# Kernel optimization log

Hardware: AMD Instinct MI355X
Metric: run time of the kernel (lower is better)

The kernel has to match this reference:

```python
import jax, jax.numpy as jnp
import numpy as np

B, T, F, H, L = 128, 256, 128, 768, 2


def lstm_cell(x, h, c, Wih, Whh, b):
    # torch gate order: i, f, g, o
    gates = x @ Wih.T + h @ Whh.T + b
    i, f, g, o = jnp.split(gates, 4, axis=-1)
    i = jax.nn.sigmoid(i)
    f = jax.nn.sigmoid(f)
    g = jnp.tanh(g)
    o = jax.nn.sigmoid(o)
    c2 = f * c + i * g
    h2 = o * jnp.tanh(c2)
    return h2, c2


def setup_inputs() -> dict:
    key = jax.random.key(0)
    ks = jax.random.split(key, 20)
    k_scale = 1.0 / np.sqrt(H)

    def U(k, shape):
        return jax.random.uniform(k, shape, jnp.float32, -k_scale, k_scale)

    inp = {
        "x": jax.random.normal(ks[0], (B, T, F), jnp.float32),
        "h0": jax.random.normal(ks[1], (L, B, H), jnp.float32),
        "c0": jax.random.normal(ks[2], (L, B, H), jnp.float32),
        # encoder LSTM (layer 0 input dim F, layer 1 input dim H); b = b_ih + b_hh fused
        "enc_Wih0": U(ks[3], (4 * H, F)),
        "enc_Whh0": U(ks[4], (4 * H, H)),
        "enc_b0": U(ks[5], (4 * H,)),
        "enc_Wih1": U(ks[6], (4 * H, H)),
        "enc_Whh1": U(ks[7], (4 * H, H)),
        "enc_b1": U(ks[8], (4 * H,)),
        # decoder LSTM
        "dec_Wih0": U(ks[9], (4 * H, F)),
        "dec_Whh0": U(ks[10], (4 * H, H)),
        "dec_b0": U(ks[11], (4 * H,)),
        "dec_Wih1": U(ks[12], (4 * H, H)),
        "dec_Whh1": U(ks[13], (4 * H, H)),
        "dec_b1": U(ks[14], (4 * H,)),
        # output projection hidden -> feature
        "lin_W": U(ks[15], (F, H)),
        "lin_b": U(ks[16], (F,)),
    }
    return inp


def reference(x, h0, c0,
              enc_Wih0, enc_Whh0, enc_b0, enc_Wih1, enc_Whh1, enc_b1,
              dec_Wih0, dec_Whh0, dec_b0, dec_Wih1, dec_Whh1, dec_b1,
              lin_W, lin_b):
    # ---- Encoder: 2-layer LSTM over full sequence, keep final (h, c) ----
    xs = jnp.transpose(x, (1, 0, 2))  # [T, B, F]

    def enc_step(carry, xt):
        (h_l0, h_l1), (c_l0, c_l1) = carry
        h0n, c0n = lstm_cell(xt, h_l0, c_l0, enc_Wih0, enc_Whh0, enc_b0)
        h1n, c1n = lstm_cell(h0n, h_l1, c_l1, enc_Wih1, enc_Whh1, enc_b1)
        return ((h0n, h1n), (c0n, c1n)), None

    enc_init = ((h0[0], h0[1]), (c0[0], c0[1]))
    (h_fin, c_fin), _ = jax.lax.scan(enc_step, enc_init, xs)

    x_dec0 = x[:, -1, :]  # [B, F]

    def dec_step(carry, _):
        (h_l0, h_l1), (c_l0, c_l1), xd = carry
        h0n, c0n = lstm_cell(xd, h_l0, c_l0, dec_Wih0, dec_Whh0, dec_b0)
        h1n, c1n = lstm_cell(h0n, h_l1, c_l1, dec_Wih1, dec_Whh1, dec_b1)
        y = h1n @ lin_W.T + lin_b  # [B, F]
        return (((h0n, h1n), (c0n, c1n), y)), y

    dec_init = (h_fin, c_fin, x_dec0)
    _, ys = jax.lax.scan(dec_step, dec_init, None, length=T)  # [T, B, F]

    # decoder step t writes output index T-1-t -> reversed time order
    out = jnp.transpose(jnp.flip(ys, axis=0), (1, 0, 2))  # [B, T, F]
    return out
```

## Files before the change

kernel.cpp:

```cpp
#include <hip/hip_runtime.h>

#define B_ 128
#define T_ 256
#define F_ 128
#define H_ 768
#define NG 3072
#define BM 32
#define BN 64
#define BK 128
#define UPT 16

typedef short s16x8 __attribute__((ext_vector_type(8)));
typedef float f32x4 __attribute__((ext_vector_type(4)));

__device__ __forceinline__ unsigned short f2bf(float x) {
  unsigned u = __float_as_uint(x);
  u += 0x7fffu + ((u >> 16) & 1u);
  return (unsigned short)(u >> 16);
}

__device__ __forceinline__ void async16(const void* g, void* l) {
  __builtin_amdgcn_global_load_lds(
      (const __attribute__((address_space(1))) void*)g,
      (__attribute__((address_space(3))) void*)l, 16, 0, 0);
}

struct Cell {
  const unsigned short* A1; int lda1; int K1;
  const unsigned short* A2; int lda2; int K2;
  const unsigned short* W;  int ldw;
  const float* bias;
  float* c;
  unsigned short* h;
  float* yout; int yt;
  int N; int ngates;
};

__global__ __launch_bounds__(256, 2) void cell_kernel(Cell ca, Cell cb, int mode)
{
  __shared__ union SM {
    struct { unsigned short A[3][BM*BK]; unsigned short Bm[3][BN*BK]; } stg;
    float gates[BM][BN+4];
  } sm;

  const int bid = (int)blockIdx.x;
  int tm, tn; bool isB = false;
  if (mode == 0) {
    int xcd = bid & 7, j = bid >> 3;
    isB = j >= 24; int jj = isB ? j - 24 : j;
    tn = xcd * 6 + (jj >> 2); tm = jj & 3;
  } else if (mode == 1) {
    int xcd = bid & 7, j = bid >> 3;
    if (j < 24) { tn = xcd * 6 + (j >> 2); tm = j & 3; }
    else        { tn = 48 + (xcd >> 2); tm = xcd & 3; }
  } else if (mode == 2) {
    int xcd = bid & 7, j = bid >> 3;
    tn = xcd * 6 + (j >> 2); tm = j & 3;
  } else {
    tm = bid & 3; tn = bid >> 2;
  }
  const Cell C = isB ? cb : ca;
  const int b0 = tm * BM;

  const int tid  = (int)threadIdx.x;
  const int wave = tid >> 6;
  const int lane = tid & 63;
  const int wm = wave >> 1, wn = wave & 1;

  const int nit = (C.K1 + C.K2) / BK;

  f32x4 acc[2] = {{0.f,0.f,0.f,0.f},{0.f,0.f,0.f,0.f}};

  auto stage = [&](int buf, int ck) {
    int kk = ck * BK;
#pragma unroll
    for (int q = 0; q < 2; ++q) {
      int cch = wave*2 + q;
      int P = cch*1024 + lane*16;
      int r = P >> 8;
      int sl = ((P >> 4) & 15) ^ (r & 7);
      int ke = kk + sl*8;
      const unsigned short* gp = (ke < C.K1)
        ? (C.A1 + (long)(b0 + r) * C.lda1 + ke)
        : (C.A2 + (long)(b0 + r) * C.lda2 + (ke - C.K1));
      async16(gp, (char*)(sm.stg.A[buf]) + cch*1024);
    }
#pragma unroll
    for (int q = 0; q < 4; ++q) {
      int cch = wave*4 + q;
      int P = cch*1024 + lane*16;
      int r = P >> 8;
      int sl = ((P >> 4) & 15) ^ (r & 7);
      int ke = kk + sl*8;
      const unsigned short* gp = C.W + (long)(tn*BN + r) * C.ldw + ke;
      async16(gp, (char*)(sm.stg.Bm[buf]) + cch*1024);
    }
  };

  auto compute = [&](int buf) {
    const char* At = (const char*)(sm.stg.A[buf]);
    const char* Bt = (const char*)(sm.stg.Bm[buf]);
#pragma unroll
    for (int ks = 0; ks < 4; ++ks) {
      int ar = wm*16 + (lane & 15);
      int as = (ks*4 + (lane >> 4)) ^ (ar & 7);
      s16x8 a = *(const s16x8*)(At + ar*256 + as*16);
#pragma unroll
      for (int nf = 0; nf < 2; ++nf) {
        int br = wn*32 + nf*16 + (lane & 15);
        int bsl = (ks*4 + (lane >> 4)) ^ (br & 7);
        s16x8 b = *(const s16x8*)(Bt + br*256 + bsl*16);
        acc[nf] = __builtin_amdgcn_mfma_f32_16x16x32_bf16(a, b, acc[nf], 0, 0, 0);
      }
    }
  };

  stage(0, 0);
  stage(1, 1);
  for (int it = 0; it < nit; ++it) {
    if (it + 1 < nit) asm volatile("s_waitcnt vmcnt(6)" ::: "memory");
    else              asm volatile("s_waitcnt vmcnt(0)" ::: "memory");
    __builtin_amdgcn_s_barrier();
    __builtin_amdgcn_sched_barrier(0);
    if (it + 2 < nit) stage((it + 2) % 3, it + 2);
    compute(it % 3);
  }

  const int gcol0 = tn * BN;
  if (gcol0 >= C.ngates) {
#pragma unroll
    for (int nf = 0; nf < 2; ++nf) {
      int col = wn*32 + nf*16 + (lane & 15);
      float bia = C.bias[gcol0 + col];
      int fo = gcol0 + col - C.ngates;
#pragma unroll
      for (int rg = 0; rg < 4; ++rg) {
        int brow = wm*16 + (lane >> 4)*4 + rg;
        C.yout[(long)(b0 + brow)*(T_*F_) + (long)C.yt*F_ + fo] = acc[nf][rg] + bia;
      }
    }
    return;
  }

  __syncthreads();
#pragma unroll
  for (int nf = 0; nf < 2; ++nf) {
    int col = wn*32 + nf*16 + (lane & 15);
#pragma unroll
    for (int rg = 0; rg < 4; ++rg) {
      int brow = wm*16 + (lane >> 4)*4 + rg;
      sm.gates[brow][col] = acc[nf][rg];
    }
  }
  __syncthreads();

  const float* bs0 = C.bias + (long)tn*BN;
  for (int e = tid; e < BM*UPT; e += 256) {
    int bl = e >> 4, ul = e & 15;
    float gi = sm.gates[bl][ 0 + ul] + bs0[ 0 + ul];
    float gf = sm.gates[bl][16 + ul] + bs0[16 + ul];
    float gg = sm.gates[bl][32 + ul] + bs0[32 + ul];
    float go = sm.gates[bl][48 + ul] + bs0[48 + ul];
    float iv = 1.f / (1.f + __expf(-gi));
    float fv = 1.f / (1.f + __expf(-gf));
    float gc = fminf(fmaxf(gg, -15.f), 15.f);
    float eg = __expf(2.f * gc);
    float gv = (eg - 1.f) / (eg + 1.f);
    float ov = 1.f / (1.f + __expf(-go));
    long ci = (long)(b0 + bl)*H_ + (long)tn*UPT + ul;
    float c2 = fv * C.c[ci] + iv * gv;
    C.c[ci] = c2;
    float cc = fminf(fmaxf(c2, -15.f), 15.f);
    float ec = __expf(2.f * cc);
    float th = (ec - 1.f) / (ec + 1.f);
    C.h[ci] = f2bf(ov * th);
  }
}

__global__ void k_convx(const float* x, unsigned short* xbf, long n) {
  long st = (long)gridDim.x * 256;
  for (long i = (long)blockIdx.x*256 + threadIdx.x; i < n; i += st) xbf[i] = f2bf(x[i]);
}

__global__ void k_init(const float* h0in, const float* c0in,
                       unsigned short* h0e0, unsigned short* h1e1,
                       float* c0buf, float* c1buf) {
  int i = blockIdx.x*256 + threadIdx.x;
  if (i < B_*H_) {
    h0e0[i] = f2bf(h0in[i]);
    h1e1[i] = f2bf(h0in[B_*H_ + i]);
    c0buf[i] = c0in[i];
    c1buf[i] = c0in[B_*H_ + i];
  }
}

__global__ __launch_bounds__(256) void k_wcomb(const float* A, const float* Bm, float* Cm) {
  __shared__ float sA[16*128];
  int tid = threadIdx.x;
  int r0 = blockIdx.x * 16;
  int c0 = blockIdx.y * 128;
  for (int e = tid; e < 16*128; e += 256)
    sA[e] = A[(long)(r0 + (e >> 7))*128 + (e & 127)];
  __syncthreads();
  int col = c0 + (tid & 127);
  int rg = (tid >> 7) * 8;
  float acc[8] = {0,0,0,0,0,0,0,0};
  for (int k = 0; k < 128; ++k) {
    float b = Bm[(long)k*768 + col];
#pragma unroll
    for (int r = 0; r < 8; ++r) acc[r] += sA[(rg + r)*128 + k] * b;
  }
  for (int r = 0; r < 8; ++r) Cm[(long)(r0 + rg + r)*768 + col] = acc[r];
}

__global__ void k_bcomb(const float* dWih0, const float* linb, const float* db0, float* bc) {
  int j = blockIdx.x*256 + threadIdx.x;
  if (j < NG) {
    float s = db0[j];
    for (int f = 0; f < 128; ++f) s += dWih0[(long)j*128 + f] * linb[f];
    bc[j] = s;
  }
}

__global__ void k_pack(unsigned short* dst, float* bdst, const float* s1, int K1,
                       const float* s2, int K2, const float* bs) {
  long Kt = K1 + K2, total = (long)NG * Kt;
  long st = (long)gridDim.x * 256;
  for (long i = (long)blockIdx.x*256 + threadIdx.x; i < total; i += st) {
    int n = (int)(i / Kt), k = (int)(i % Kt);
    int tn = n >> 6, r = n & 63;
    int j = (r >> 4)*H_ + tn*UPT + (r & 15);
    float v = (k < K1) ? s1[(long)j*K1 + k] : s2[(long)j*K2 + (k - K1)];
    dst[i] = f2bf(v);
    if (k == 0) bdst[n] = bs[j];
  }
}

__global__ void k_packext(unsigned short* dst, float* bdst, const float* wcomb,
                          const float* whh0, const float* bcomb,
                          const float* linW, const float* linb) {
  long total = (long)(NG + F_) * (2*H_);
  long st = (long)gridDim.x * 256;
  for (long i = (long)blockIdx.x*256 + threadIdx.x; i < total; i += st) {
    int n = (int)(i / (2*H_)), k = (int)(i % (2*H_));
    float v;
    if (n < NG) {
      int tn = n >> 6, r = n & 63;
      int j = (r >> 4)*H_ + tn*UPT + (r & 15);
      v = (k < H_) ? wcomb[(long)j*H_ + k] : whh0[(long)j*H_ + (k - H_)];
      if (k == 0) bdst[n] = bcomb[j];
    } else {
      int f = n - NG;
      v = (k < H_) ? linW[(long)f*H_ + k] : 0.f;
      if (k == 0) bdst[n] = linb[f];
    }
    dst[i] = f2bf(v);
  }
}

__global__ void k_packlin(unsigned short* dst, const float* linW) {
  int i = blockIdx.x*256 + threadIdx.x;
  if (i < F_*H_) dst[i] = f2bf(linW[i]);
}

extern "C" void kernel_launch(void* const* d_in, const int* in_sizes, int n_in,
                              void* d_out, int out_size, void* d_ws, size_t ws_size,
                              hipStream_t stream)
{
  (void)in_sizes; (void)n_in; (void)out_size; (void)ws_size;
  const float* x     = (const float*)d_in[0];
  const float* h0in  = (const float*)d_in[1];
  const float* c0in  = (const float*)d_in[2];
  const float* eWih0 = (const float*)d_in[3];
  const float* eWhh0 = (const float*)d_in[4];
  const float* eb0   = (const float*)d_in[5];
  const float* eWih1 = (const float*)d_in[6];
  const float* eWhh1 = (const float*)d_in[7];
  const float* eb1   = (const float*)d_in[8];
  const float* dWih0 = (const float*)d_in[9];
  const float* dWhh0 = (const float*)d_in[10];
  const float* db0   = (const float*)d_in[11];
  const float* dWih1 = (const float*)d_in[12];
  const float* dWhh1 = (const float*)d_in[13];
  const float* db1   = (const float*)d_in[14];
  const float* linW  = (const float*)d_in[15];
  const float* linb  = (const float*)d_in[16];
  float* out = (float*)d_out;

  char* wp = (char*)d_ws;
  auto alloc = [&](size_t bytes) -> void* {
    void* p = (void*)wp;
    wp += (bytes + 255) & ~(size_t)255;
    return p;
  };
  unsigned short* xbf    = (unsigned short*)alloc((size_t)B_*T_*F_*2);
  unsigned short* Wenc0  = (unsigned short*)alloc((size_t)NG*(F_+H_)*2);
  unsigned short* Wenc1  = (unsigned short*)alloc((size_t)NG*(2*H_)*2);
  unsigned short* Wdec0f = (unsigned short*)alloc((size_t)NG*(F_+H_)*2);
  unsigned short* Wext   = (unsigned short*)alloc((size_t)(NG+F_)*(2*H_)*2);
  unsigned short* Wdec1  = (unsigned short*)alloc((size_t)NG*(2*H_)*2);
  unsigned short* linWbf = (unsigned short*)alloc((size_t)F_*H_*2);
  float* Wcomb = (float*)alloc((size_t)NG*H_*4);
  float* benc0 = (float*)alloc((size_t)NG*4);
  float* benc1 = (float*)alloc((size_t)NG*4);
  float* bdec0f= (float*)alloc((size_t)NG*4);
  float* bext  = (float*)alloc((size_t)(NG+F_)*4);
  float* bdec1 = (float*)alloc((size_t)NG*4);
  float* bcomb = (float*)alloc((size_t)NG*4);
  unsigned short* h0e[2];
  h0e[0] = (unsigned short*)alloc((size_t)B_*H_*2);
  h0e[1] = (unsigned short*)alloc((size_t)B_*H_*2);
  unsigned short* h1e[2];
  h1e[0] = (unsigned short*)alloc((size_t)B_*H_*2);
  h1e[1] = (unsigned short*)alloc((size_t)B_*H_*2);
  float* c0buf = (float*)alloc((size_t)B_*H_*4);
  float* c1buf = (float*)alloc((size_t)B_*H_*4);

  k_convx<<<2048, 256, 0, stream>>>(x, xbf, (long)B_*T_*F_);
  k_init<<<(B_*H_+255)/256, 256, 0, stream>>>(h0in, c0in, h0e[0], h1e[1], c0buf, c1buf);
  k_wcomb<<<dim3(192,6), 256, 0, stream>>>(dWih0, linW, Wcomb);
  k_bcomb<<<(NG+255)/256, 256, 0, stream>>>(dWih0, linb, db0, bcomb);
  k_pack<<<2048, 256, 0, stream>>>(Wenc0, benc0, eWih0, F_, eWhh0, H_, eb0);
  k_pack<<<2048, 256, 0, stream>>>(Wenc1, benc1, eWih1, H_, eWhh1, H_, eb1);
  k_pack<<<2048, 256, 0, stream>>>(Wdec0f, bdec0f, dWih0, F_, dWhh0, H_, db0);
  k_pack<<<2048, 256, 0, stream>>>(Wdec1, bdec1, dWih1, H_, dWhh1, H_, db1);
  k_packext<<<2048, 256, 0, stream>>>(Wext, bext, Wcomb, dWhh0, bcomb, linW, linb);
  k_packlin<<<(F_*H_+255)/256, 256, 0, stream>>>(linWbf, linW);

  auto mk = [&](const unsigned short* A1, int lda1, int K1,
                const unsigned short* A2, int lda2, int K2,
                const unsigned short* W, const float* bias,
                float* c, unsigned short* h, float* yo, int yt,
                int N, int ngates) {
    Cell cc; cc.A1=A1; cc.lda1=lda1; cc.K1=K1; cc.A2=A2; cc.lda2=lda2; cc.K2=K2;
    cc.W=W; cc.ldw=K1+K2; cc.bias=bias; cc.c=c; cc.h=h; cc.yout=yo; cc.yt=yt;
    cc.N=N; cc.ngates=ngates;
    return cc;
  };

  for (int s = 0; s <= T_; ++s) {
    Cell cA = {}, cB = {};
    bool hasA = (s < T_), hasB = (s >= 1);
    if (hasA)
      cA = mk(xbf + (long)s*F_, T_*F_, F_, h0e[s&1], H_, H_,
              Wenc0, benc0, c0buf, h0e[(s+1)&1], nullptr, 0, NG, NG);
    if (hasB)
      cB = mk(h0e[s&1], H_, H_, h1e[s&1], H_, H_,
              Wenc1, benc1, c1buf, h1e[(s+1)&1], nullptr, 0, NG, NG);
    if (hasA && hasB) cell_kernel<<<384, 256, 0, stream>>>(cA, cB, 0);
    else if (hasA)    cell_kernel<<<192, 256, 0, stream>>>(cA, cA, 2);
    else              cell_kernel<<<192, 256, 0, stream>>>(cB, cB, 2);
  }

  {
    Cell c0 = mk(xbf + (long)(T_-1)*F_, T_*F_, F_, h0e[0], H_, H_,
                 Wdec0f, bdec0f, c0buf, h0e[1], nullptr, 0, NG, NG);
    cell_kernel<<<192, 256, 0, stream>>>(c0, c0, 2);
    Cell c1 = mk(h0e[1], H_, H_, h1e[1], H_, H_,
                 Wdec1, bdec1, c1buf, h1e[0], nullptr, 0, NG, NG);
    cell_kernel<<<192, 256, 0, stream>>>(c1, c1, 2);
  }
  for (int t = 1; t < T_; ++t) {
    Cell cd0 = mk(h1e[(t+1)&1], H_, H_, h0e[t&1], H_, H_,
                  Wext, bext, c0buf, h0e[(t+1)&1], out, T_-t, NG+F_, NG);
    cell_kernel<<<200, 256, 0, stream>>>(cd0, cd0, 1);
    Cell cd1 = mk(h0e[(t+1)&1], H_, H_, h1e[(t+1)&1], H_, H_,
                  Wdec1, bdec1, c1buf, h1e[t&1], nullptr, 0, NG, NG);
    cell_kernel<<<192, 256, 0, stream>>>(cd1, cd1, 2);
  }
  {
    Cell cy = mk(h1e[1], H_, H_, h1e[1], H_, 0,
                 linWbf, linb, nullptr, nullptr, out, 0, F_, 0);
    cell_kernel<<<8, 256, 0, stream>>>(cy, cy, 3);
  }
}
```

Measured before the change: 7.206 ms.

## Fuse decoder layer-0 and layer-1 cells into one launch with flag-based sync

Decoder timesteps now launch a single kernel in which layer-1 blocks spin-wait on per-tile flags written by layer-0 blocks, instead of two separate kernel launches. This targets per-step launch overhead and the gap between kernels. The A operand is now fully preloaded into LDS at the start. The approach relies on layer-0 blocks being scheduled before waiting blocks occupy the GPU, and adds spin polling plus a timeout abort path that could produce wrong output if it fires.

```diff
diff --git a/kernel.cpp b/kernel.cpp
--- a/kernel.cpp
+++ b/kernel.cpp
@@ -36,7 +36,54 @@
   int N; int ngates;
 };
 
-__global__ __launch_bounds__(256, 2) void cell_kernel(Cell ca, Cell cb, int mode)
+__device__ __forceinline__ void compute_frag(const char* At, const char* Bt,
+                                             f32x4 acc[2], int wm, int wn, int lane) {
+#pragma unroll
+  for (int ks = 0; ks < 4; ++ks) {
+    int ar = wm*16 + (lane & 15);
+    int as = (ks*4 + (lane >> 4)) ^ (ar & 7);
+    s16x8 a = *(const s16x8*)(At + ar*256 + as*16);
+#pragma unroll
+    for (int nf = 0; nf < 2; ++nf) {
+      int br = wn*32 + nf*16 + (lane & 15);
+      int bsl = (ks*4 + (lane >> 4)) ^ (br & 7);
+      s16x8 b = *(const s16x8*)(Bt + br*256 + bsl*16);
+      acc[nf] = __builtin_amdgcn_mfma_f32_16x16x32_bf16(a, b, acc[nf], 0, 0, 0);
+    }
+  }
+}
+
+__device__ bool waitN(int* fl, int count, int* abortf, int* sres, int tid) {
+  if (tid == 0) *sres = 1;
+  __syncthreads();
+  bool ok = true;
+  if (tid < count) {
+    if (__hip_atomic_load(fl + tid, __ATOMIC_RELAXED, __HIP_MEMORY_SCOPE_AGENT) == 0) {
+      int n = 0;
+      for (;;) {
+        if (__hip_atomic_load(fl + tid, __ATOMIC_RELAXED, __HIP_MEMORY_SCOPE_AGENT) != 0) break;
+        __builtin_amdgcn_s_sleep(2);
+        if ((++n & 63) == 0) {
+          if (__hip_atomic_load(abortf, __ATOMIC_RELAXED, __HIP_MEMORY_SCOPE_AGENT)) { ok = false; break; }
+          if (n > 400000) {
+            __hip_atomic_store(abortf, 1, __ATOMIC_RELAXED, __HIP_MEMORY_SCOPE_AGENT);
+            ok = false; break;
+          }
+        }
+      }
+    }
+    if (ok) (void)__hip_atomic_load(fl + tid, __ATOMIC_ACQUIRE, __HIP_MEMORY_SCOPE_AGENT);
+  }
+  if (!ok) *sres = 0;
+  __syncthreads();
+  return *sres != 0;
+}
+
+__device__ __forceinline__ void postf(int* fl) {
+  __hip_atomic_store(fl, 1, __ATOMIC_RELEASE, __HIP_MEMORY_SCOPE_AGENT);
+}
+
+__global__ __launch_bounds__(256, 2) void enc_kernel(Cell ca, Cell cb, int mode)
 {
   __shared__ union SM {
     struct { unsigned short A[3][BM*BK]; unsigned short Bm[3][BN*BK]; } stg;
@@ -49,10 +96,6 @@
     int xcd = bid & 7, j = bid >> 3;
     isB = j >= 24; int jj = isB ? j - 24 : j;
     tn = xcd * 6 + (jj >> 2); tm = jj & 3;
-  } else if (mode == 1) {
-    int xcd = bid & 7, j = bid >> 3;
-    if (j < 24) { tn = xcd * 6 + (j >> 2); tm = j & 3; }
-    else        { tn = 48 + (xcd >> 2); tm = xcd & 3; }
   } else if (mode == 2) {
     int xcd = bid & 7, j = bid >> 3;
     tn = xcd * 6 + (j >> 2); tm = j & 3;
@@ -97,24 +140,6 @@
     }
   };
 
-  auto compute = [&](int buf) {
-    const char* At = (const char*)(sm.stg.A[buf]);
-    const char* Bt = (const char*)(sm.stg.Bm[buf]);
-#pragma unroll
-    for (int ks = 0; ks < 4; ++ks) {
-      int ar = wm*16 + (lane & 15);
-      int as = (ks*4 + (lane >> 4)) ^ (ar & 7);
-      s16x8 a = *(const s16x8*)(At + ar*256 + as*16);
-#pragma unroll
-      for (int nf = 0; nf < 2; ++nf) {
-        int br = wn*32 + nf*16 + (lane & 15);
-        int bsl = (ks*4 + (lane >> 4)) ^ (br & 7);
-        s16x8 b = *(const s16x8*)(Bt + br*256 + bsl*16);
-        acc[nf] = __builtin_amdgcn_mfma_f32_16x16x32_bf16(a, b, acc[nf], 0, 0, 0);
-      }
-    }
-  };
-
   stage(0, 0);
   stage(1, 1);
   for (int it = 0; it < nit; ++it) {
@@ -123,7 +148,8 @@
     __builtin_amdgcn_s_barrier();
     __builtin_amdgcn_sched_barrier(0);
     if (it + 2 < nit) stage((it + 2) % 3, it + 2);
-    compute(it % 3);
+    compute_frag((const char*)sm.stg.A[it % 3], (const char*)sm.stg.Bm[it % 3],
+                 acc, wm, wn, lane);
   }
 
   const int gcol0 = tn * BN;
@@ -174,6 +200,132 @@
     float ec = __expf(2.f * cc);
     float th = (ec - 1.f) / (ec + 1.f);
     C.h[ci] = f2bf(ov * th);
+  }
+}
+
+__global__ __launch_bounds__(256, 1) void dec_kernel(Cell ca, Cell cb, int n0,
+                                                     int* fl, int* abortf)
+{
+  __shared__ union SMD {
+    struct { char A[12][8192]; char Bm[3][16384]; } s;
+    float gates[BM][BN+4];
+  } sm;
+  __shared__ int sres;
+
+  const int bid = (int)blockIdx.x;
+  const int tid = (int)threadIdx.x;
+  const int wave = tid >> 6, lane = tid & 63;
+  const int wm = wave >> 1, wn = wave & 1;
+
+  const bool isB = bid >= n0;
+  int tm, tn;
+  if (!isB) {
+    int xcd = bid & 7, j = bid >> 3;
+    if (j < 24) { tn = xcd*6 + (j >> 2); tm = j & 3; }
+    else        { tn = 48 + (xcd >> 2); tm = xcd & 3; }
+  } else {
+    int i = bid - n0;
+    int xcd = i & 7, j = i >> 3;
+    tn = xcd*6 + (j >> 2); tm = j & 3;
+  }
+  const Cell C = isB ? cb : ca;
+  const int b0 = tm * BM;
+  const int nit = (C.K1 + C.K2) / BK;
+
+  if (isB) { if (!waitN(fl, 192, abortf, &sres, tid)) return; }
+
+  for (int c0 = 0; c0 < nit; ++c0) {
+    int kk = c0 * BK;
+#pragma unroll
+    for (int q = 0; q < 2; ++q) {
+      int cch = wave*2 + q;
+      int P = cch*1024 + lane*16;
+      int r = P >> 8;
+      int sl = ((P >> 4) & 15) ^ (r & 7);
+      int ke = kk + sl*8;
+      const unsigned short* gp = (ke < C.K1)
+        ? (C.A1 + (long)(b0 + r) * C.lda1 + ke)
+        : (C.A2 + (long)(b0 + r) * C.lda2 + (ke - C.K1));
+      async16(gp, sm.s.A[c0] + cch*1024);
+    }
+  }
+  auto stageB = [&](int buf, int ck) {
+    int kk = ck * BK;
+#pragma unroll
+    for (int q = 0; q < 4; ++q) {
+      int cch = wave*4 + q;
+      int P = cch*1024 + lane*16;
+      int r = P >> 8;
+      int sl = ((P >> 4) & 15) ^ (r & 7);
+      int ke = kk + sl*8;
+      async16(C.W + (long)(tn*BN + r) * C.ldw + ke, sm.s.Bm[buf] + cch*1024);
+    }
+  };
+  stageB(0, 0);
+  stageB(1, 1);
+
+  f32x4 acc[2] = {{0.f,0.f,0.f,0.f},{0.f,0.f,0.f,0.f}};
+  for (int it = 0; it < nit; ++it) {
+    if (it + 1 < nit) asm volatile("s_waitcnt vmcnt(4)" ::: "memory");
+    else              asm volatile("s_waitcnt vmcnt(0)" ::: "memory");
+    __builtin_amdgcn_s_barrier();
+    __builtin_amdgcn_sched_barrier(0);
+    if (it + 2 < nit) stageB((it + 2) % 3, it + 2);
+    compute_frag(sm.s.A[it], sm.s.Bm[it % 3], acc, wm, wn, lane);
+  }
+
+  const int gcol0 = tn * BN;
+  if (gcol0 >= C.ngates) {
+#pragma unroll
+    for (int nf = 0; nf < 2; ++nf) {
+      int col = wn*32 + nf*16 + (lane & 15);
+      float bia = C.bias[gcol0 + col];
+      int fo = gcol0 + col - C.ngates;
+#pragma unroll
+      for (int rg = 0; rg < 4; ++rg) {
+        int brow = wm*16 + (lane >> 4)*4 + rg;
+        C.yout[(long)(b0 + brow)*(T_*F_) + (long)C.yt*F_ + fo] = acc[nf][rg] + bia;
+      }
+    }
+    return;
+  }
+
+  __syncthreads();
+#pragma unroll
+  for (int nf = 0; nf < 2; ++nf) {
+    int col = wn*32 + nf*16 + (lane & 15);
+#pragma unroll
+    for (int rg = 0; rg < 4; ++rg) {
+      int brow = wm*16 + (lane >> 4)*4 + rg;
+      sm.gates[brow][col] = acc[nf][rg];
+    }
+  }
+  __syncthreads();
+
+  const float* bs0 = C.bias + (long)tn*BN;
+  for (int e = tid; e < BM*UPT; e += 256) {
+    int bl = e >> 4, ul = e & 15;
+    float gi = sm.gates[bl][ 0 + ul] + bs0[ 0 + ul];
+    float gf = sm.gates[bl][16 + ul] + bs0[16 + ul];
+    float gg = sm.gates[bl][32 + ul] + bs0[32 + ul];
+    float go = sm.gates[bl][48 + ul] + bs0[48 + ul];
+    float iv = 1.f / (1.f + __expf(-gi));
+    float fv = 1.f / (1.f + __expf(-gf));
+    float gc = fminf(fmaxf(gg, -15.f), 15.f);
+    float eg = __expf(2.f * gc);
+    float gv = (eg - 1.f) / (eg + 1.f);
+    float ov = 1.f / (1.f + __expf(-go));
+    long ci = (long)(b0 + bl)*H_ + (long)tn*UPT + ul;
+    float c2 = fv * C.c[ci] + iv * gv;
+    C.c[ci] = c2;
+    float cc = fminf(fmaxf(c2, -15.f), 15.f);
+    float ec = __expf(2.f * cc);
+    float th = (ec - 1.f) / (ec + 1.f);
+    C.h[ci] = f2bf(ov * th);
+  }
+  if (!isB) {
+    __syncthreads();
+    if (tid == 0) postf(fl + tn*4 + tm);
   }
 }
 
@@ -293,6 +445,8 @@
     wp += (bytes + 255) & ~(size_t)255;
     return p;
   };
+  int* flags = (int*)alloc((size_t)(256*192 + 1) * 4);
+  int* abortf = flags + 256*192;
   unsigned short* xbf    = (unsigned short*)alloc((size_t)B_*T_*F_*2);
   unsigned short* Wenc0  = (unsigned short*)alloc((size_t)NG*(F_+H_)*2);
   unsigned short* Wenc1  = (unsigned short*)alloc((size_t)NG*(2*H_)*2);
@@ -316,6 +470,8 @@
   float* c0buf = (float*)alloc((size_t)B_*H_*4);
   float* c1buf = (float*)alloc((size_t)B_*H_*4);
 
+  hipMemsetAsync(flags, 0, (size_t)(256*192 + 1) * 4, stream);
+
   k_convx<<<2048, 256, 0, stream>>>(x, xbf, (long)B_*T_*F_);
   k_init<<<(B_*H_+255)/256, 256, 0, stream>>>(h0in, c0in, h0e[0], h1e[1], c0buf, c1buf);
   k_wcomb<<<dim3(192,6), 256, 0, stream>>>(dWih0, linW, Wcomb);
@@ -347,30 +503,28 @@
     if (hasB)
       cB = mk(h0e[s&1], H_, H_, h1e[s&1], H_, H_,
               Wenc1, benc1, c1buf, h1e[(s+1)&1], nullptr, 0, NG, NG);
-    if (hasA && hasB) cell_kernel<<<384, 256, 0, stream>>>(cA, cB, 0);
-    else if (hasA)    cell_kernel<<<192, 256, 0, stream>>>(cA, cA, 2);
-    else              cell_kernel<<<192, 256, 0, stream>>>(cB, cB, 2);
+    if (hasA && hasB) enc_kernel<<<384, 256, 0, stream>>>(cA, cB, 0);
+    else if (hasA)    enc_kernel<<<192, 256, 0, stream>>>(cA, cA, 2);
+    else              enc_kernel<<<192, 256, 0, stream>>>(cB, cB, 2);
   }
 
   {
-    Cell c0 = mk(xbf + (long)(T_-1)*F_, T_*F_, F_, h0e[0], H_, H_,
-                 Wdec0f, bdec0f, c0buf, h0e[1], nullptr, 0, NG, NG);
-    cell_kernel<<<192, 256, 0, stream>>>(c0, c0, 2);
-    Cell c1 = mk(h0e[1], H_, H_, h1e[1], H_, H_,
-                 Wdec1, bdec1, c1buf, h1e[0], nullptr, 0, NG, NG);
-    cell_kernel<<<192, 256, 0, stream>>>(c1, c1, 2);
+    Cell c0f = mk(xbf + (long)(T_-1)*F_, T_*F_, F_, h0e[0], H_, H_,
+                  Wdec0f, bdec0f, c0buf, h0e[1], nullptr, 0, NG, NG);
+    Cell c10 = mk(h0e[1], H_, H_, h1e[1], H_, H_,
+                  Wdec1, bdec1, c1buf, h1e[0], nullptr, 0, NG, NG);
+    dec_kernel<<<384, 256, 0, stream>>>(c0f, c10, 192, flags + 0, abortf);
   }
   for (int t = 1; t < T_; ++t) {
     Cell cd0 = mk(h1e[(t+1)&1], H_, H_, h0e[t&1], H_, H_,
                   Wext, bext, c0buf, h0e[(t+1)&1], out, T_-t, NG+F_, NG);
-    cell_kernel<<<200, 256, 0, stream>>>(cd0, cd0, 1);
     Cell cd1 = mk(h0e[(t+1)&1], H_, H_, h1e[(t+1)&1], H_, H_,
                   Wdec1, bdec1, c1buf, h1e[t&1], nullptr, 0, NG, NG);
-    cell_kernel<<<192, 256, 0, stream>>>(cd1, cd1, 2);
+    dec_kernel<<<392, 256, 0, stream>>>(cd0, cd1, 200, flags + (long)t*192, abortf);
   }
   {
     Cell cy = mk(h1e[1], H_, H_, h1e[1], H_, 0,
                  linWbf, linb, nullptr, nullptr, out, 0, F_, 0);
-    cell_kernel<<<8, 256, 0, stream>>>(cy, cy, 3);
-  }
-}
+    enc_kernel<<<8, 256, 0, stream>>>(cy, cy, 3);
+  }
+}
```

After: 10.49 ms. 1.46x slower.

## Split decoder recurrent GEMMs into partial sums computed one step ahead

Applied to the files above, without the earlier changes.

Splits each decoder cell GEMM so that the recurrent-hidden part (h_prev @ Whh) is computed ahead of time into a partial-sum buffer. That work runs in the same launch as the previous cell's finishing GEMM, and the finishing kernel then adds the partial sums in its epilogue. Each launch now does only half-K work on the critical path, and two independent halves share one grid, halving dependent K depth per step. The cost is extra fp32 partial-buffer traffic, an extra LDS buffer, and more intricate ping-pong buffer indexing across steps.

```diff
diff --git a/kernel.cpp b/kernel.cpp
--- a/kernel.cpp
+++ b/kernel.cpp
@@ -26,38 +26,44 @@
 }
 
 struct Cell {
-  const unsigned short* A1; int lda1; int K1;
-  const unsigned short* A2; int lda2; int K2;
+  const unsigned short* A1; long lda1; int K1;
+  const unsigned short* A2; long lda2; int K2;
   const unsigned short* W;  int ldw;
   const float* bias;
   float* c;
   unsigned short* h;
   float* yout; int yt;
-  int N; int ngates;
+  const float* pin;
+  float* pout;
+  int ngates;
 };
 
-__global__ __launch_bounds__(256, 2) void cell_kernel(Cell ca, Cell cb, int mode)
+__global__ __launch_bounds__(256, 2) void cell_kernel(Cell ca, Cell cb, int na, int modeA)
 {
   __shared__ union SM {
     struct { unsigned short A[3][BM*BK]; unsigned short Bm[3][BN*BK]; } stg;
     float gates[BM][BN+4];
   } sm;
+  __shared__ float part[BM][BN];
 
   const int bid = (int)blockIdx.x;
-  int tm, tn; bool isB = false;
-  if (mode == 0) {
-    int xcd = bid & 7, j = bid >> 3;
-    isB = j >= 24; int jj = isB ? j - 24 : j;
-    tn = xcd * 6 + (jj >> 2); tm = jj & 3;
-  } else if (mode == 1) {
-    int xcd = bid & 7, j = bid >> 3;
-    if (j < 24) { tn = xcd * 6 + (j >> 2); tm = j & 3; }
-    else        { tn = 48 + (xcd >> 2); tm = xcd & 3; }
-  } else if (mode == 2) {
-    int xcd = bid & 7, j = bid >> 3;
-    tn = xcd * 6 + (j >> 2); tm = j & 3;
+  const bool isB = bid >= na;
+  int tm, tn;
+  if (!isB) {
+    if (modeA == 1) {
+      int xcd = bid & 7, j = bid >> 3;
+      if (j < 24) { tn = xcd*6 + (j >> 2); tm = j & 3; }
+      else        { tn = 48 + (xcd >> 2); tm = xcd & 3; }
+    } else if (modeA == 3) {
+      tm = bid & 3; tn = bid >> 2;
+    } else {
+      int xcd = bid & 7, j = bid >> 3;
+      tn = xcd*6 + (j >> 2); tm = j & 3;
+    }
   } else {
-    tm = bid & 3; tn = bid >> 2;
+    int i = bid - na;
+    int xcd = i & 7, j = i >> 3;
+    tn = xcd*6 + (j >> 2); tm = j & 3;
   }
   const Cell C = isB ? cb : ca;
   const int b0 = tm * BM;
@@ -68,6 +74,9 @@
   const int wm = wave >> 1, wn = wave & 1;
 
   const int nit = (C.K1 + C.K2) / BK;
+  const int gcol0 = tn * BN;
+  const float* pin = (C.pin != nullptr && gcol0 < C.ngates && C.pout == nullptr)
+                   ? (C.pin + ((long)tn*128 + b0)*64) : nullptr;
 
   f32x4 acc[2] = {{0.f,0.f,0.f,0.f},{0.f,0.f,0.f,0.f}};
 
@@ -97,36 +106,54 @@
     }
   };
 
-  auto compute = [&](int buf) {
-    const char* At = (const char*)(sm.stg.A[buf]);
-    const char* Bt = (const char*)(sm.stg.Bm[buf]);
-#pragma unroll
-    for (int ks = 0; ks < 4; ++ks) {
-      int ar = wm*16 + (lane & 15);
-      int as = (ks*4 + (lane >> 4)) ^ (ar & 7);
-      s16x8 a = *(const s16x8*)(At + ar*256 + as*16);
-#pragma unroll
-      for (int nf = 0; nf < 2; ++nf) {
-        int br = wn*32 + nf*16 + (lane & 15);
-        int bsl = (ks*4 + (lane >> 4)) ^ (br & 7);
-        s16x8 b = *(const s16x8*)(Bt + br*256 + bsl*16);
-        acc[nf] = __builtin_amdgcn_mfma_f32_16x16x32_bf16(a, b, acc[nf], 0, 0, 0);
-      }
-    }
-  };
-
+  if (pin) {
+#pragma unroll
+    for (int q = 0; q < 2; ++q) {
+      int ch = wave*2 + q;
+      async16(pin + ch*256 + lane*4, (char*)part + ch*1024);
+    }
+  }
   stage(0, 0);
-  stage(1, 1);
+  if (nit > 1) stage(1, 1);
   for (int it = 0; it < nit; ++it) {
     if (it + 1 < nit) asm volatile("s_waitcnt vmcnt(6)" ::: "memory");
     else              asm volatile("s_waitcnt vmcnt(0)" ::: "memory");
     __builtin_amdgcn_s_barrier();
     __builtin_amdgcn_sched_barrier(0);
     if (it + 2 < nit) stage((it + 2) % 3, it + 2);
-    compute(it % 3);
-  }
-
-  const int gcol0 = tn * BN;
+    {
+      const char* At = (const char*)(sm.stg.A[it % 3]);
+      const char* Bt = (const char*)(sm.stg.Bm[it % 3]);
+#pragma unroll
+      for (int ks = 0; ks < 4; ++ks) {
+        int ar = wm*16 + (lane & 15);
+        int as = (ks*4 + (lane >> 4)) ^ (ar & 7);
+        s16x8 a = *(const s16x8*)(At + ar*256 + as*16);
+#pragma unroll
+        for (int nf = 0; nf < 2; ++nf) {
+          int br = wn*32 + nf*16 + (lane & 15);
+          int bsl = (ks*4 + (lane >> 4)) ^ (br & 7);
+          s16x8 b = *(const s16x8*)(Bt + br*256 + bsl*16);
+          acc[nf] = __builtin_amdgcn_mfma_f32_16x16x32_bf16(a, b, acc[nf], 0, 0, 0);
+        }
+      }
+    }
+  }
+
+  if (C.pout) {
+    float* po = C.pout + ((long)tn*128 + b0)*64;
+#pragma unroll
+    for (int nf = 0; nf < 2; ++nf) {
+      int col = wn*32 + nf*16 + (lane & 15);
+#pragma unroll
+      for (int rg = 0; rg < 4; ++rg) {
+        int brow = wm*16 + (lane >> 4)*4 + rg;
+        po[(long)brow*64 + col] = acc[nf][rg];
+      }
+    }
+    return;
+  }
+
   if (gcol0 >= C.ngates) {
 #pragma unroll
     for (int nf = 0; nf < 2; ++nf) {
@@ -161,6 +188,12 @@
     float gf = sm.gates[bl][16 + ul] + bs0[16 + ul];
     float gg = sm.gates[bl][32 + ul] + bs0[32 + ul];
     float go = sm.gates[bl][48 + ul] + bs0[48 + ul];
+    if (pin) {
+      gi += part[bl][ 0 + ul];
+      gf += part[bl][16 + ul];
+      gg += part[bl][32 + ul];
+      go += part[bl][48 + ul];
+    }
     float iv = 1.f / (1.f + __expf(-gi));
     float fv = 1.f / (1.f + __expf(-gf));
     float gc = fminf(fmaxf(gg, -15.f), 15.f);
@@ -307,6 +340,8 @@
   float* bext  = (float*)alloc((size_t)(NG+F_)*4);
   float* bdec1 = (float*)alloc((size_t)NG*4);
   float* bcomb = (float*)alloc((size_t)NG*4);
+  float* p0buf = (float*)alloc((size_t)48*128*64*4);
+  float* p1buf = (float*)alloc((size_t)48*128*64*4);
   unsigned short* h0e[2];
   h0e[0] = (unsigned short*)alloc((size_t)B_*H_*2);
   h0e[1] = (unsigned short*)alloc((size_t)B_*H_*2);
@@ -327,50 +362,79 @@
   k_packext<<<2048, 256, 0, stream>>>(Wext, bext, Wcomb, dWhh0, bcomb, linW, linb);
   k_packlin<<<(F_*H_+255)/256, 256, 0, stream>>>(linWbf, linW);
 
-  auto mk = [&](const unsigned short* A1, int lda1, int K1,
-                const unsigned short* A2, int lda2, int K2,
-                const unsigned short* W, const float* bias,
+  auto mk = [&](const unsigned short* A1, long lda1, int K1,
+                const unsigned short* A2, long lda2, int K2,
+                const unsigned short* W, int ldw, const float* bias,
                 float* c, unsigned short* h, float* yo, int yt,
-                int N, int ngates) {
+                const float* pin, float* pout, int ngates) {
     Cell cc; cc.A1=A1; cc.lda1=lda1; cc.K1=K1; cc.A2=A2; cc.lda2=lda2; cc.K2=K2;
-    cc.W=W; cc.ldw=K1+K2; cc.bias=bias; cc.c=c; cc.h=h; cc.yout=yo; cc.yt=yt;
-    cc.N=N; cc.ngates=ngates;
+    cc.W=W; cc.ldw=ldw; cc.bias=bias; cc.c=c; cc.h=h; cc.yout=yo; cc.yt=yt;
+    cc.pin=pin; cc.pout=pout; cc.ngates=ngates;
     return cc;
   };
 
-  for (int s = 0; s <= T_; ++s) {
-    Cell cA = {}, cB = {};
-    bool hasA = (s < T_), hasB = (s >= 1);
-    if (hasA)
-      cA = mk(xbf + (long)s*F_, T_*F_, F_, h0e[s&1], H_, H_,
-              Wenc0, benc0, c0buf, h0e[(s+1)&1], nullptr, 0, NG, NG);
-    if (hasB)
-      cB = mk(h0e[s&1], H_, H_, h1e[s&1], H_, H_,
-              Wenc1, benc1, c1buf, h1e[(s+1)&1], nullptr, 0, NG, NG);
-    if (hasA && hasB) cell_kernel<<<384, 256, 0, stream>>>(cA, cB, 0);
-    else if (hasA)    cell_kernel<<<192, 256, 0, stream>>>(cA, cA, 2);
-    else              cell_kernel<<<192, 256, 0, stream>>>(cB, cB, 2);
-  }
-
+  for (int s = 0; s < T_; ++s) {
+    Cell cA = mk(xbf + (long)s*F_, (long)T_*F_, F_, h0e[s&1], H_, H_,
+                 Wenc0, F_+H_, benc0, c0buf, h0e[(s+1)&1], nullptr, 0,
+                 nullptr, nullptr, NG);
+    if (s == 0) {
+      cell_kernel<<<192, 256, 0, stream>>>(cA, cA, 192, 2);
+    } else {
+      Cell cB = mk(h0e[s&1], H_, H_, h1e[s&1], H_, H_,
+                   Wenc1, 2*H_, benc1, c1buf, h1e[(s+1)&1], nullptr, 0,
+                   nullptr, nullptr, NG);
+      cell_kernel<<<384, 256, 0, stream>>>(cA, cB, 192, 2);
+    }
+  }
   {
-    Cell c0 = mk(xbf + (long)(T_-1)*F_, T_*F_, F_, h0e[0], H_, H_,
-                 Wdec0f, bdec0f, c0buf, h0e[1], nullptr, 0, NG, NG);
-    cell_kernel<<<192, 256, 0, stream>>>(c0, c0, 2);
-    Cell c1 = mk(h0e[1], H_, H_, h1e[1], H_, H_,
-                 Wdec1, bdec1, c1buf, h1e[0], nullptr, 0, NG, NG);
-    cell_kernel<<<192, 256, 0, stream>>>(c1, c1, 2);
+    Cell cB = mk(h0e[0], H_, H_, h1e[0], H_, H_,
+                 Wenc1, 2*H_, benc1, c1buf, h1e[1], nullptr, 0,
+                 nullptr, nullptr, NG);
+    Cell cP = mk(h0e[0], H_, H_, nullptr, 0, 0,
+                 Wdec0f + F_, F_+H_, nullptr, nullptr, nullptr, nullptr, 0,
+                 nullptr, p0buf, NG);
+    cell_kernel<<<384, 256, 0, stream>>>(cB, cP, 192, 2);
+  }
+
+  {
+    Cell cF = mk(xbf + (long)(T_-1)*F_, (long)T_*F_, F_, nullptr, 0, 0,
+                 Wdec0f, F_+H_, bdec0f, c0buf, h0e[1], nullptr, 0,
+                 p0buf, nullptr, NG);
+    Cell cP = mk(h1e[1], H_, H_, nullptr, 0, 0,
+                 Wdec1 + H_, 2*H_, nullptr, nullptr, nullptr, nullptr, 0,
+                 nullptr, p1buf, NG);
+    cell_kernel<<<384, 256, 0, stream>>>(cF, cP, 192, 2);
   }
   for (int t = 1; t < T_; ++t) {
-    Cell cd0 = mk(h1e[(t+1)&1], H_, H_, h0e[t&1], H_, H_,
-                  Wext, bext, c0buf, h0e[(t+1)&1], out, T_-t, NG+F_, NG);
-    cell_kernel<<<200, 256, 0, stream>>>(cd0, cd0, 1);
-    Cell cd1 = mk(h0e[(t+1)&1], H_, H_, h1e[(t+1)&1], H_, H_,
-                  Wdec1, bdec1, c1buf, h1e[t&1], nullptr, 0, NG, NG);
-    cell_kernel<<<192, 256, 0, stream>>>(cd1, cd1, 2);
+    {
+      Cell cF = mk(h0e[t&1], H_, H_, nullptr, 0, 0,
+                   Wdec1, 2*H_, bdec1, c1buf, h1e[(t-1)&1], nullptr, 0,
+                   p1buf, nullptr, NG);
+      Cell cP = mk(h0e[t&1], H_, H_, nullptr, 0, 0,
+                   Wext + H_, 2*H_, nullptr, nullptr, nullptr, nullptr, 0,
+                   nullptr, p0buf, NG);
+      cell_kernel<<<384, 256, 0, stream>>>(cF, cP, 192, 2);
+    }
+    {
+      Cell cF = mk(h1e[(t+1)&1], H_, H_, nullptr, 0, 0,
+                   Wext, 2*H_, bext, c0buf, h0e[(t+1)&1], out, T_-t,
+                   p0buf, nullptr, NG);
+      Cell cP = mk(h1e[(t+1)&1], H_, H_, nullptr, 0, 0,
+                   Wdec1 + H_, 2*H_, nullptr, nullptr, nullptr, nullptr, 0,
+                   nullptr, p1buf, NG);
+      cell_kernel<<<392, 256, 0, stream>>>(cF, cP, 200, 1);
+    }
   }
   {
-    Cell cy = mk(h1e[1], H_, H_, h1e[1], H_, 0,
-                 linWbf, linb, nullptr, nullptr, out, 0, F_, 0);
-    cell_kernel<<<8, 256, 0, stream>>>(cy, cy, 3);
-  }
-}
+    Cell cF = mk(h0e[0], H_, H_, nullptr, 0, 0,
+                 Wdec1, 2*H_, bdec1, c1buf, h1e[1], nullptr, 0,
+                 p1buf, nullptr, NG);
+    cell_kernel<<<192, 256, 0, stream>>>(cF, cF, 192, 2);
+  }
+  {
+    Cell cy = mk(h1e[1], H_, H_, nullptr, 0, 0,
+                 linWbf, H_, linb, nullptr, nullptr, out, 0,
+                 nullptr, nullptr, 0);
+    cell_kernel<<<8, 256, 0, stream>>>(cy, cy, 8, 3);
+  }
+}
```

Result: slower. 9.559 ms (+32.7%).
